# Performance work log

Measured on AMD Instinct MI355X. Metric: run time of the kernel, lower is better.

The kernel has to match this reference:

```python
import jax, jax.numpy as jnp
import numpy as np

NEG_INF = -9e15
LEAKY_SLOPE = 0.01  # PyTorch F.leaky_relu default


def setup_inputs() -> dict:
    key = jax.random.key(0)
    k1, k2, k3, k4 = jax.random.split(key, 4)
    B, N, Fin, Fout = 4, 4096, 64, 64
    X = jax.random.normal(k1, (B, N, Fin), dtype=jnp.float32)
    A = jax.random.randint(k2, (N, N), 0, 2, dtype=jnp.int32)
    weight = jax.random.normal(k3, (Fin, Fout), dtype=jnp.float32) * 0.15
    a = jax.random.normal(k4, (2 * Fout, 1), dtype=jnp.float32) * 0.15
    return {"X": X, "A": A, "weight": weight, "a": a}


def reference(X, A, weight, a):
    B, N, _ = X.shape
    Fout = weight.shape[1]
    # add self loops: A[i,i] = 1
    mask = (A > 0) | jnp.eye(N, dtype=bool)  # [N, N]
    Xw = jnp.matmul(X, weight)  # [B, N, Fout]
    # additive attention: e_ij = leaky_relu(a_l . x_i + a_r . x_j)
    # equivalent to the repeat/cat/matmul in the original, without O(N^2 F) memory
    a_l = a[:Fout, 0]   # [Fout]
    a_r = a[Fout:, 0]   # [Fout]
    left = jnp.einsum('bnf,f->bn', Xw, a_l)   # [B, N]
    right = jnp.einsum('bnf,f->bn', Xw, a_r)  # [B, N]
    e = left[:, :, None] + right[:, None, :]  # [B, N, N]
    e = jnp.where(e >= 0, e, LEAKY_SLOPE * e)
    att = jnp.where(mask[None, :, :], e, NEG_INF)
    att = jax.nn.softmax(att, axis=-1)  # dropout p=0 -> identity
    out = jnp.matmul(att, Xw)  # [B, N, Fout]
    return out
```

## Files before the change

kernel.cpp:

```cpp
#include <hip/hip_runtime.h>
#include <hip/hip_bf16.h>
#include <math.h>

#define BB 4
#define NN 4096
#define FF 64
#define KS (NN / 32)
#define NKW (KS / 4)
#define C0F 3.35462628e-4f
#define C1F 3.35462628e-6f
#define PREB 512

typedef _Float16 half8 __attribute__((ext_vector_type(8)));
typedef float f32x4 __attribute__((ext_vector_type(4)));

__global__ __launch_bounds__(256, 2)
void k_prep(const float* __restrict__ X, const float* __restrict__ W,
            const float* __restrict__ avec, const int* __restrict__ A,
            _Float16* __restrict__ XwP, float2* __restrict__ LE,
            float* __restrict__ ERt, float* __restrict__ RCt,
            unsigned int* __restrict__ bitsT) {
    __shared__ __align__(16) float Wl[64 * 64];
    __shared__ __align__(16) float Xl[32][64];
    __shared__ __align__(16) float T[32][65];
    __shared__ float al[64];
    __shared__ float ar[64];

    const int t = threadIdx.x;

    if (blockIdx.x >= PREB) {
        int pidx = (blockIdx.x - PREB) * 256 + t;
        int row  = pidx >> 10;
        int c4   = pidx & 1023;
        const uint4* A4 = (const uint4*)A;
        uint4 av = A4[pidx];
        unsigned int nib = 0;
        nib |= ((int)av.x > 0) ? 1u : 0u;
        nib |= ((int)av.y > 0) ? 2u : 0u;
        nib |= ((int)av.z > 0) ? 4u : 0u;
        nib |= ((int)av.w > 0) ? 8u : 0u;
        if (c4 == (row >> 2)) nib |= 1u << (row & 3);
        int lane = t & 63;
        unsigned int v = nib << ((lane & 7) * 4);
        v |= __shfl_xor(v, 1);
        v |= __shfl_xor(v, 2);
        v |= __shfl_xor(v, 4);
        if ((lane & 7) == 0)
            bitsT[(size_t)(c4 >> 3) * NN + row] = v;
        return;
    }

    const int lane = t & 63;
    const int wv = t >> 6;
    const int r0 = blockIdx.x * 32;

    #pragma unroll
    for (int k = 0; k < 16; ++k) Wl[t + k * 256] = W[t + k * 256];
    if (t < 64) { al[t] = avec[t]; ar[t] = avec[64 + t]; }
    {
        const float4* xs = (const float4*)(X + (size_t)r0 * 64);
        float4* xd = (float4*)&Xl[0][0];
        xd[t] = xs[t];
        xd[t + 256] = xs[t + 256];
    }
    __syncthreads();

    float Wreg[64];
    #pragma unroll
    for (int k = 0; k < 64; ++k) Wreg[k] = Wl[k * 64 + lane];

    #pragma unroll
    for (int rr = 0; rr < 8; ++rr) {
        int lrow = wv * 8 + rr;
        int row  = r0 + lrow;
        float a0 = 0.f, a1 = 0.f, a2 = 0.f, a3 = 0.f;
        #pragma unroll
        for (int k = 0; k < 64; k += 4) {
            float4 x = *(const float4*)&Xl[lrow][k];
            a0 = fmaf(x.x, Wreg[k],     a0);
            a1 = fmaf(x.y, Wreg[k + 1], a1);
            a2 = fmaf(x.z, Wreg[k + 2], a2);
            a3 = fmaf(x.w, Wreg[k + 3], a3);
        }
        float acc = (a0 + a1) + (a2 + a3);
        T[lrow][lane] = acc;

        float lv = acc * al[lane];
        float rv = acc * ar[lane];
        #pragma unroll
        for (int off = 32; off; off >>= 1) {
            lv += __shfl_xor(lv, off, 64);
            rv += __shfl_xor(rv, off, 64);
        }
        if (lane == 0) {
            LE[row]  = make_float2(lv * C1F, __expf(lv - 8.f));
            ERt[row] = __expf(rv);
            RCt[row] = fmaf(rv, C1F, C0F);
        }
    }
    __syncthreads();

    int b  = r0 >> 12;
    int ks = (r0 & (NN - 1)) >> 5;
    int ct = t >> 6;
    int q  = lane >> 4, n = lane & 15;
    half8 h;
    #pragma unroll
    for (int jj = 0; jj < 8; ++jj)
        h[jj] = (_Float16)T[q * 8 + jj][ct * 16 + n];
    *(half8*)&XwP[((((size_t)b * KS + ks) * 4 + ct) * 64 + lane) * 8] = h;
}

__global__ __launch_bounds__(256, 2)
void k_main(const _Float16* __restrict__ XwP, const float2* __restrict__ LE,
            const float* __restrict__ ERt, const float* __restrict__ RCt,
            const unsigned int* __restrict__ bitsT, float* __restrict__ out) {
    __shared__ __align__(16) char smem[32768];
    __shared__ uint2 lutm[16];
    float* REs_er = (float*)smem;
    float* REs_rc = (float*)(smem + 16384);
    float (*Lacc)[32][68] = (float (*)[32][68])smem;
    float* Lsum = (float*)(smem + 17408);

    const int t  = threadIdx.x;
    const int b  = blockIdx.y;
    const int i0 = blockIdx.x * 32;

    const int lane = t & 63;
    const int wv   = t >> 6;
    const int lm   = lane & 15;
    const int q    = lane >> 4;

    const int rowa = i0 + lm;
    const int rowb = i0 + 16 + lm;
    const float2 lea = LE[b * NN + rowa];
    const float2 leb = LE[b * NN + rowb];
    const _Float16* xp = XwP + (size_t)b * KS * 2048 + (size_t)lane * 8;

    if (t < 16)
        lutm[t] = make_uint2(((t & 1) ? 0xFFFFu : 0u) | ((t & 2) ? 0xFFFF0000u : 0u),
                             ((t & 4) ? 0xFFFFu : 0u) | ((t & 8) ? 0xFFFF0000u : 0u));

    {
        const float4* es = (const float4*)(ERt + (size_t)b * NN);
        const float4* cs = (const float4*)(RCt + (size_t)b * NN);
        float4* ed = (float4*)REs_er;
        float4* cd = (float4*)REs_rc;
        #pragma unroll
        for (int k = 0; k < 4; ++k) {
            ed[t + k * 256] = es[t + k * 256];
            cd[t + k * 256] = cs[t + k * 256];
        }
    }
    __syncthreads();

    f32x4 acca[4], accb[4];
    f32x4 sacca = (f32x4)0.f, saccb = (f32x4)0.f;
    #pragma unroll
    for (int ct = 0; ct < 4; ++ct) { acca[ct] = (f32x4)0.f; accb[ct] = (f32x4)0.f; }
    half8 vones;
    #pragma unroll
    for (int k = 0; k < 8; ++k) vones[k] = (_Float16)1.0f;

    const int ks0 = wv * NKW;

    const _Float16* base = xp + (size_t)ks0 * 2048;
    half8 nb0 = *(const half8*)(base + 0 * 512);
    half8 nb1 = *(const half8*)(base + 1 * 512);
    half8 nb2 = *(const half8*)(base + 2 * 512);
    half8 nb3 = *(const half8*)(base + 3 * 512);
    unsigned int nwa = bitsT[(size_t)ks0 * NN + rowa];
    unsigned int nwb = bitsT[(size_t)ks0 * NN + rowb];

    #pragma unroll 4
    for (int kk = 0; kk < NKW; ++kk) {
        half8 bf0 = nb0, bf1 = nb1, bf2 = nb2, bf3 = nb3;
        unsigned int wax = nwa >> (q * 8);
        unsigned int wbx = nwb >> (q * 8);
        uint2 ma0 = lutm[wax & 15], ma1 = lutm[(wax >> 4) & 15];
        uint2 mb0 = lutm[wbx & 15], mb1 = lutm[(wbx >> 4) & 15];

        {
            int nk = kk + 1 < NKW ? kk + 1 : kk;
            const _Float16* nbase = xp + (size_t)(ks0 + nk) * 2048;
            nb0 = *(const half8*)(nbase + 0 * 512);
            nb1 = *(const half8*)(nbase + 1 * 512);
            nb2 = *(const half8*)(nbase + 2 * 512);
            nb3 = *(const half8*)(nbase + 3 * 512);
            nwa = bitsT[(size_t)(ks0 + nk) * NN + rowa];
            nwb = bitsT[(size_t)(ks0 + nk) * NN + rowb];
        }

        const float4* ep = (const float4*)(REs_er + (ks0 + kk) * 32 + q * 8);
        float4 e0v = ep[0], e1v = ep[1];
        const float4* cp = (const float4*)(REs_rc + (ks0 + kk) * 32 + q * 8);
        float4 c0v = cp[0], c1v = cp[1];
        float er8[8] = {e0v.x, e0v.y, e0v.z, e0v.w, e1v.x, e1v.y, e1v.z, e1v.w};
        float rc8[8] = {c0v.x, c0v.y, c0v.z, c0v.w, c1v.x, c1v.y, c1v.z, c1v.w};

        float pa[8], pb[8];
        #pragma unroll
        for (int jj = 0; jj < 8; ++jj)
            pa[jj] = fmaxf(lea.y * er8[jj], lea.x + rc8[jj]);
        #pragma unroll
        for (int jj = 0; jj < 8; ++jj)
            pb[jj] = fmaxf(leb.y * er8[jj], leb.x + rc8[jj]);

        uint4 ua, ub;
        ua.x = __builtin_bit_cast(unsigned int, __builtin_amdgcn_cvt_pkrtz(pa[0], pa[1])) & ma0.x;
        ua.y = __builtin_bit_cast(unsigned int, __builtin_amdgcn_cvt_pkrtz(pa[2], pa[3])) & ma0.y;
        ua.z = __builtin_bit_cast(unsigned int, __builtin_amdgcn_cvt_pkrtz(pa[4], pa[5])) & ma1.x;
        ua.w = __builtin_bit_cast(unsigned int, __builtin_amdgcn_cvt_pkrtz(pa[6], pa[7])) & ma1.y;
        ub.x = __builtin_bit_cast(unsigned int, __builtin_amdgcn_cvt_pkrtz(pb[0], pb[1])) & mb0.x;
        ub.y = __builtin_bit_cast(unsigned int, __builtin_amdgcn_cvt_pkrtz(pb[2], pb[3])) & mb0.y;
        ub.z = __builtin_bit_cast(unsigned int, __builtin_amdgcn_cvt_pkrtz(pb[4], pb[5])) & mb1.x;
        ub.w = __builtin_bit_cast(unsigned int, __builtin_amdgcn_cvt_pkrtz(pb[6], pb[7])) & mb1.y;
        half8 a0a = __builtin_bit_cast(half8, ua);
        half8 a0b = __builtin_bit_cast(half8, ub);

        __builtin_amdgcn_s_setprio(1);
        acca[0] = __builtin_amdgcn_mfma_f32_16x16x32_f16(a0a, bf0, acca[0], 0, 0, 0);
        acca[1] = __builtin_amdgcn_mfma_f32_16x16x32_f16(a0a, bf1, acca[1], 0, 0, 0);
        acca[2] = __builtin_amdgcn_mfma_f32_16x16x32_f16(a0a, bf2, acca[2], 0, 0, 0);
        acca[3] = __builtin_amdgcn_mfma_f32_16x16x32_f16(a0a, bf3, acca[3], 0, 0, 0);
        sacca   = __builtin_amdgcn_mfma_f32_16x16x32_f16(a0a, vones, sacca, 0, 0, 0);

        accb[0] = __builtin_amdgcn_mfma_f32_16x16x32_f16(a0b, bf0, accb[0], 0, 0, 0);
        accb[1] = __builtin_amdgcn_mfma_f32_16x16x32_f16(a0b, bf1, accb[1], 0, 0, 0);
        accb[2] = __builtin_amdgcn_mfma_f32_16x16x32_f16(a0b, bf2, accb[2], 0, 0, 0);
        accb[3] = __builtin_amdgcn_mfma_f32_16x16x32_f16(a0b, bf3, accb[3], 0, 0, 0);
        saccb   = __builtin_amdgcn_mfma_f32_16x16x32_f16(a0b, vones, saccb, 0, 0, 0);
        __builtin_amdgcn_s_setprio(0);
    }

    __syncthreads();

    if (wv >= 2) {
        #pragma unroll
        for (int r = 0; r < 4; ++r) {
            int lrow = q * 4 + r;
            #pragma unroll
            for (int ct = 0; ct < 4; ++ct) {
                Lacc[wv - 2][lrow][ct * 16 + lm]      = acca[ct][r];
                Lacc[wv - 2][16 + lrow][ct * 16 + lm] = accb[ct][r];
            }
            if (lm == 0) {
                Lsum[(wv - 2) * 32 + lrow]      = sacca[r];
                Lsum[(wv - 2) * 32 + 16 + lrow] = saccb[r];
            }
        }
    }
    __syncthreads();
    if (wv < 2) {
        #pragma unroll
        for (int r = 0; r < 4; ++r) {
            int lrow = q * 4 + r;
            #pragma unroll
            for (int ct = 0; ct < 4; ++ct) {
                Lacc[wv][lrow][ct * 16 + lm]      += acca[ct][r];
                Lacc[wv][16 + lrow][ct * 16 + lm] += accb[ct][r];
            }
            if (lm == 0) {
                Lsum[wv * 32 + lrow]      += sacca[r];
                Lsum[wv * 32 + 16 + lrow] += saccb[r];
            }
        }
    }
    __syncthreads();
    #pragma unroll
    for (int it = 0; it < 2; ++it) {
        int idx  = t + it * 256;
        int lrow = idx >> 4;
        int c0   = (idx & 15) * 4;
        float s = Lsum[lrow] + Lsum[32 + lrow];
        float inv = 1.f / s;
        float4 o;
        o.x = (Lacc[0][lrow][c0 + 0] + Lacc[1][lrow][c0 + 0]) * inv;
        o.y = (Lacc[0][lrow][c0 + 1] + Lacc[1][lrow][c0 + 1]) * inv;
        o.z = (Lacc[0][lrow][c0 + 2] + Lacc[1][lrow][c0 + 2]) * inv;
        o.w = (Lacc[0][lrow][c0 + 3] + Lacc[1][lrow][c0 + 3]) * inv;
        *(float4*)&out[((size_t)(b * NN + i0 + lrow) << 6) + c0] = o;
    }
}

extern "C" void kernel_launch(void* const* d_in, const int* in_sizes, int n_in,
                              void* d_out, int out_size, void* d_ws, size_t ws_size,
                              hipStream_t stream) {
    const float* X    = (const float*)d_in[0];
    const int*   A    = (const int*)d_in[1];
    const float* W    = (const float*)d_in[2];
    const float* avec = (const float*)d_in[3];
    float* out = (float*)d_out;

    char* ws = (char*)d_ws;
    size_t off = 0;
    _Float16* XwP = (_Float16*)(ws + off); off += (size_t)BB * NN * FF * 2;
    float2* LE = (float2*)(ws + off);      off += (size_t)BB * NN * 8;
    float* ERt = (float*)(ws + off);       off += (size_t)BB * NN * 4;
    float* RCt = (float*)(ws + off);       off += (size_t)BB * NN * 4;
    unsigned int* bitsT = (unsigned int*)(ws + off);
    off += (size_t)KS * NN * 4;
    (void)off; (void)ws_size;

    k_prep<<<PREB + NN * NN / 1024, 256, 0, stream>>>(X, W, avec, A, XwP, LE, ERt, RCt, bitsT);
    k_main<<<dim3(NN / 32, BB), 256, 0, stream>>>(XwP, LE, ERt, RCt, bitsT, out);
}
```

Baseline: 125.6 us.

## Process 64 rows per block to reuse XwP B-fragments across four row groups

```diff
diff --git a/kernel.cpp b/kernel.cpp
--- a/kernel.cpp
+++ b/kernel.cpp
@@ -111,30 +111,33 @@
     *(half8*)&XwP[((((size_t)b * KS + ks) * 4 + ct) * 64 + lane) * 8] = h;
 }
 
-__global__ __launch_bounds__(256, 2)
+__global__ __launch_bounds__(256, 1)
 void k_main(const _Float16* __restrict__ XwP, const float2* __restrict__ LE,
             const float* __restrict__ ERt, const float* __restrict__ RCt,
             const unsigned int* __restrict__ bitsT, float* __restrict__ out) {
-    __shared__ __align__(16) char smem[32768];
+    __shared__ __align__(16) char smem[35840];
     __shared__ uint2 lutm[16];
     float* REs_er = (float*)smem;
     float* REs_rc = (float*)(smem + 16384);
-    float (*Lacc)[32][68] = (float (*)[32][68])smem;
-    float* Lsum = (float*)(smem + 17408);
+    float (*Lacc)[64][68] = (float (*)[64][68])smem;
+    float* Lsum = (float*)(smem + 34816);
 
     const int t  = threadIdx.x;
     const int b  = blockIdx.y;
-    const int i0 = blockIdx.x * 32;
+    const int i0 = blockIdx.x * 64;
 
     const int lane = t & 63;
     const int wv   = t >> 6;
     const int lm   = lane & 15;
     const int q    = lane >> 4;
 
-    const int rowa = i0 + lm;
-    const int rowb = i0 + 16 + lm;
-    const float2 lea = LE[b * NN + rowa];
-    const float2 leb = LE[b * NN + rowb];
+    int rowg[4];
+    float2 le[4];
+    #pragma unroll
+    for (int g = 0; g < 4; ++g) {
+        rowg[g] = i0 + g * 16 + lm;
+        le[g]   = LE[b * NN + rowg[g]];
+    }
     const _Float16* xp = XwP + (size_t)b * KS * 2048 + (size_t)lane * 8;
 
     if (t < 16)
@@ -154,10 +157,14 @@
     }
     __syncthreads();
 
-    f32x4 acca[4], accb[4];
-    f32x4 sacca = (f32x4)0.f, saccb = (f32x4)0.f;
-    #pragma unroll
-    for (int ct = 0; ct < 4; ++ct) { acca[ct] = (f32x4)0.f; accb[ct] = (f32x4)0.f; }
+    f32x4 acc[4][4];
+    f32x4 sacc[4];
+    #pragma unroll
+    for (int g = 0; g < 4; ++g) {
+        sacc[g] = (f32x4)0.f;
+        #pragma unroll
+        for (int ct = 0; ct < 4; ++ct) acc[g][ct] = (f32x4)0.f;
+    }
     half8 vones;
     #pragma unroll
     for (int k = 0; k < 8; ++k) vones[k] = (_Float16)1.0f;
@@ -169,16 +176,16 @@
     half8 nb1 = *(const half8*)(base + 1 * 512);
     half8 nb2 = *(const half8*)(base + 2 * 512);
     half8 nb3 = *(const half8*)(base + 3 * 512);
-    unsigned int nwa = bitsT[(size_t)ks0 * NN + rowa];
-    unsigned int nwb = bitsT[(size_t)ks0 * NN + rowb];
-
-    #pragma unroll 4
+    unsigned int nw[4];
+    #pragma unroll
+    for (int g = 0; g < 4; ++g) nw[g] = bitsT[(size_t)ks0 * NN + rowg[g]];
+
+    #pragma unroll 2
     for (int kk = 0; kk < NKW; ++kk) {
         half8 bf0 = nb0, bf1 = nb1, bf2 = nb2, bf3 = nb3;
-        unsigned int wax = nwa >> (q * 8);
-        unsigned int wbx = nwb >> (q * 8);
-        uint2 ma0 = lutm[wax & 15], ma1 = lutm[(wax >> 4) & 15];
-        uint2 mb0 = lutm[wbx & 15], mb1 = lutm[(wbx >> 4) & 15];
+        unsigned int wx[4];
+        #pragma unroll
+        for (int g = 0; g < 4; ++g) wx[g] = nw[g] >> (q * 8);
 
         {
             int nk = kk + 1 < NKW ? kk + 1 : kk;
@@ -187,8 +194,9 @@
             nb1 = *(const half8*)(nbase + 1 * 512);
             nb2 = *(const half8*)(nbase + 2 * 512);
             nb3 = *(const half8*)(nbase + 3 * 512);
-            nwa = bitsT[(size_t)(ks0 + nk) * NN + rowa];
-            nwb = bitsT[(size_t)(ks0 + nk) * NN + rowb];
+            #pragma unroll
+            for (int g = 0; g < 4; ++g)
+                nw[g] = bitsT[(size_t)(ks0 + nk) * NN + rowg[g]];
         }
 
         const float4* ep = (const float4*)(REs_er + (ks0 + kk) * 32 + q * 8);
@@ -198,81 +206,64 @@
         float er8[8] = {e0v.x, e0v.y, e0v.z, e0v.w, e1v.x, e1v.y, e1v.z, e1v.w};
         float rc8[8] = {c0v.x, c0v.y, c0v.z, c0v.w, c1v.x, c1v.y, c1v.z, c1v.w};
 
-        float pa[8], pb[8];
-        #pragma unroll
-        for (int jj = 0; jj < 8; ++jj)
-            pa[jj] = fmaxf(lea.y * er8[jj], lea.x + rc8[jj]);
-        #pragma unroll
-        for (int jj = 0; jj < 8; ++jj)
-            pb[jj] = fmaxf(leb.y * er8[jj], leb.x + rc8[jj]);
-
-        uint4 ua, ub;
-        ua.x = __builtin_bit_cast(unsigned int, __builtin_amdgcn_cvt_pkrtz(pa[0], pa[1])) & ma0.x;
-        ua.y = __builtin_bit_cast(unsigned int, __builtin_amdgcn_cvt_pkrtz(pa[2], pa[3])) & ma0.y;
-        ua.z = __builtin_bit_cast(unsigned int, __builtin_amdgcn_cvt_pkrtz(pa[4], pa[5])) & ma1.x;
-        ua.w = __builtin_bit_cast(unsigned int, __builtin_amdgcn_cvt_pkrtz(pa[6], pa[7])) & ma1.y;
-        ub.x = __builtin_bit_cast(unsigned int, __builtin_amdgcn_cvt_pkrtz(pb[0], pb[1])) & mb0.x;
-        ub.y = __builtin_bit_cast(unsigned int, __builtin_amdgcn_cvt_pkrtz(pb[2], pb[3])) & mb0.y;
-        ub.z = __builtin_bit_cast(unsigned int, __builtin_amdgcn_cvt_pkrtz(pb[4], pb[5])) & mb1.x;
-        ub.w = __builtin_bit_cast(unsigned int, __builtin_amdgcn_cvt_pkrtz(pb[6], pb[7])) & mb1.y;
-        half8 a0a = __builtin_bit_cast(half8, ua);
-        half8 a0b = __builtin_bit_cast(half8, ub);
-
-        __builtin_amdgcn_s_setprio(1);
-        acca[0] = __builtin_amdgcn_mfma_f32_16x16x32_f16(a0a, bf0, acca[0], 0, 0, 0);
-        acca[1] = __builtin_amdgcn_mfma_f32_16x16x32_f16(a0a, bf1, acca[1], 0, 0, 0);
-        acca[2] = __builtin_amdgcn_mfma_f32_16x16x32_f16(a0a, bf2, acca[2], 0, 0, 0);
-        acca[3] = __builtin_amdgcn_mfma_f32_16x16x32_f16(a0a, bf3, acca[3], 0, 0, 0);
-        sacca   = __builtin_amdgcn_mfma_f32_16x16x32_f16(a0a, vones, sacca, 0, 0, 0);
-
-        accb[0] = __builtin_amdgcn_mfma_f32_16x16x32_f16(a0b, bf0, accb[0], 0, 0, 0);
-        accb[1] = __builtin_amdgcn_mfma_f32_16x16x32_f16(a0b, bf1, accb[1], 0, 0, 0);
-        accb[2] = __builtin_amdgcn_mfma_f32_16x16x32_f16(a0b, bf2, accb[2], 0, 0, 0);
-        accb[3] = __builtin_amdgcn_mfma_f32_16x16x32_f16(a0b, bf3, accb[3], 0, 0, 0);
-        saccb   = __builtin_amdgcn_mfma_f32_16x16x32_f16(a0b, vones, saccb, 0, 0, 0);
-        __builtin_amdgcn_s_setprio(0);
+        #pragma unroll
+        for (int g = 0; g < 4; ++g) {
+            uint2 m0 = lutm[wx[g] & 15], m1 = lutm[(wx[g] >> 4) & 15];
+            float p[8];
+            #pragma unroll
+            for (int jj = 0; jj < 8; ++jj)
+                p[jj] = fmaxf(le[g].y * er8[jj], le[g].x + rc8[jj]);
+            uint4 u;
+            u.x = __builtin_bit_cast(unsigned int, __builtin_amdgcn_cvt_pkrtz(p[0], p[1])) & m0.x;
+            u.y = __builtin_bit_cast(unsigned int, __builtin_amdgcn_cvt_pkrtz(p[2], p[3])) & m0.y;
+            u.z = __builtin_bit_cast(unsigned int, __builtin_amdgcn_cvt_pkrtz(p[4], p[5])) & m1.x;
+            u.w = __builtin_bit_cast(unsigned int, __builtin_amdgcn_cvt_pkrtz(p[6], p[7])) & m1.y;
+            half8 af = __builtin_bit_cast(half8, u);
+
+            acc[g][0] = __builtin_amdgcn_mfma_f32_16x16x32_f16(af, bf0, acc[g][0], 0, 0, 0);
+            acc[g][1] = __builtin_amdgcn_mfma_f32_16x16x32_f16(af, bf1, acc[g][1], 0, 0, 0);
+            acc[g][2] = __builtin_amdgcn_mfma_f32_16x16x32_f16(af, bf2, acc[g][2], 0, 0, 0);
+            acc[g][3] = __builtin_amdgcn_mfma_f32_16x16x32_f16(af, bf3, acc[g][3], 0, 0, 0);
+            sacc[g]   = __builtin_amdgcn_mfma_f32_16x16x32_f16(af, vones, sacc[g], 0, 0, 0);
+        }
     }
 
     __syncthreads();
 
     if (wv >= 2) {
         #pragma unroll
-        for (int r = 0; r < 4; ++r) {
-            int lrow = q * 4 + r;
-            #pragma unroll
-            for (int ct = 0; ct < 4; ++ct) {
-                Lacc[wv - 2][lrow][ct * 16 + lm]      = acca[ct][r];
-                Lacc[wv - 2][16 + lrow][ct * 16 + lm] = accb[ct][r];
+        for (int g = 0; g < 4; ++g) {
+            #pragma unroll
+            for (int r = 0; r < 4; ++r) {
+                int lrow = g * 16 + q * 4 + r;
+                #pragma unroll
+                for (int ct = 0; ct < 4; ++ct)
+                    Lacc[wv - 2][lrow][ct * 16 + lm] = acc[g][ct][r];
+                if (lm == 0) Lsum[(wv - 2) * 64 + lrow] = sacc[g][r];
             }
-            if (lm == 0) {
-                Lsum[(wv - 2) * 32 + lrow]      = sacca[r];
-                Lsum[(wv - 2) * 32 + 16 + lrow] = saccb[r];
+        }
+    }
+    __syncthreads();
+    if (wv < 2) {
+        #pragma unroll
+        for (int g = 0; g < 4; ++g) {
+            #pragma unroll
+            for (int r = 0; r < 4; ++r) {
+                int lrow = g * 16 + q * 4 + r;
+                #pragma unroll
+                for (int ct = 0; ct < 4; ++ct)
+                    Lacc[wv][lrow][ct * 16 + lm] += acc[g][ct][r];
+                if (lm == 0) Lsum[wv * 64 + lrow] += sacc[g][r];
             }
         }
     }
     __syncthreads();
-    if (wv < 2) {
-        #pragma unroll
-        for (int r = 0; r < 4; ++r) {
-            int lrow = q * 4 + r;
-            #pragma unroll
-            for (int ct = 0; ct < 4; ++ct) {
-                Lacc[wv][lrow][ct * 16 + lm]      += acca[ct][r];
-                Lacc[wv][16 + lrow][ct * 16 + lm] += accb[ct][r];
-            }
-            if (lm == 0) {
-                Lsum[wv * 32 + lrow]      += sacca[r];
-                Lsum[wv * 32 + 16 + lrow] += saccb[r];
-            }
-        }
-    }
-    __syncthreads();
-    #pragma unroll
-    for (int it = 0; it < 2; ++it) {
+    #pragma unroll
+    for (int it = 0; it < 4; ++it) {
         int idx  = t + it * 256;
         int lrow = idx >> 4;
         int c0   = (idx & 15) * 4;
-        float s = Lsum[lrow] + Lsum[32 + lrow];
+        float s = Lsum[lrow] + Lsum[64 + lrow];
         float inv = 1.f / s;
         float4 o;
         o.x = (Lacc[0][lrow][c0 + 0] + Lacc[1][lrow][c0 + 0]) * inv;
@@ -303,5 +294,5 @@
     (void)off; (void)ws_size;
 
     k_prep<<<PREB + NN * NN / 1024, 256, 0, stream>>>(X, W, avec, A, XwP, LE, ERt, RCt, bitsT);
-    k_main<<<dim3(NN / 32, BB), 256, 0, stream>>>(XwP, LE, ERt, RCt, bitsT, out);
+    k_main<<<dim3(NN / 64, BB), 256, 0, stream>>>(XwP, LE, ERt, RCt, bitsT, out);
 }
```

Result: slower. 133.5 us (+6.3%).

## Deepen software pipeline to two-stage ping-pong prefetch in attention MFMA loop

Applied to the files above, without the earlier changes.

```diff
diff --git a/kernel.cpp b/kernel.cpp
--- a/kernel.cpp
+++ b/kernel.cpp
@@ -164,74 +164,101 @@
 
     const int ks0 = wv * NKW;
 
-    const _Float16* base = xp + (size_t)ks0 * 2048;
-    half8 nb0 = *(const half8*)(base + 0 * 512);
-    half8 nb1 = *(const half8*)(base + 1 * 512);
-    half8 nb2 = *(const half8*)(base + 2 * 512);
-    half8 nb3 = *(const half8*)(base + 3 * 512);
-    unsigned int nwa = bitsT[(size_t)ks0 * NN + rowa];
-    unsigned int nwb = bitsT[(size_t)ks0 * NN + rowb];
-
-    #pragma unroll 4
-    for (int kk = 0; kk < NKW; ++kk) {
-        half8 bf0 = nb0, bf1 = nb1, bf2 = nb2, bf3 = nb3;
-        unsigned int wax = nwa >> (q * 8);
-        unsigned int wbx = nwb >> (q * 8);
-        uint2 ma0 = lutm[wax & 15], ma1 = lutm[(wax >> 4) & 15];
-        uint2 mb0 = lutm[wbx & 15], mb1 = lutm[(wbx >> 4) & 15];
-
-        {
-            int nk = kk + 1 < NKW ? kk + 1 : kk;
-            const _Float16* nbase = xp + (size_t)(ks0 + nk) * 2048;
-            nb0 = *(const half8*)(nbase + 0 * 512);
-            nb1 = *(const half8*)(nbase + 1 * 512);
-            nb2 = *(const half8*)(nbase + 2 * 512);
-            nb3 = *(const half8*)(nbase + 3 * 512);
-            nwa = bitsT[(size_t)(ks0 + nk) * NN + rowa];
-            nwb = bitsT[(size_t)(ks0 + nk) * NN + rowb];
-        }
-
-        const float4* ep = (const float4*)(REs_er + (ks0 + kk) * 32 + q * 8);
-        float4 e0v = ep[0], e1v = ep[1];
-        const float4* cp = (const float4*)(REs_rc + (ks0 + kk) * 32 + q * 8);
-        float4 c0v = cp[0], c1v = cp[1];
-        float er8[8] = {e0v.x, e0v.y, e0v.z, e0v.w, e1v.x, e1v.y, e1v.z, e1v.w};
-        float rc8[8] = {c0v.x, c0v.y, c0v.z, c0v.w, c1v.x, c1v.y, c1v.z, c1v.w};
-
-        float pa[8], pb[8];
-        #pragma unroll
-        for (int jj = 0; jj < 8; ++jj)
-            pa[jj] = fmaxf(lea.y * er8[jj], lea.x + rc8[jj]);
-        #pragma unroll
-        for (int jj = 0; jj < 8; ++jj)
-            pb[jj] = fmaxf(leb.y * er8[jj], leb.x + rc8[jj]);
-
-        uint4 ua, ub;
-        ua.x = __builtin_bit_cast(unsigned int, __builtin_amdgcn_cvt_pkrtz(pa[0], pa[1])) & ma0.x;
-        ua.y = __builtin_bit_cast(unsigned int, __builtin_amdgcn_cvt_pkrtz(pa[2], pa[3])) & ma0.y;
-        ua.z = __builtin_bit_cast(unsigned int, __builtin_amdgcn_cvt_pkrtz(pa[4], pa[5])) & ma1.x;
-        ua.w = __builtin_bit_cast(unsigned int, __builtin_amdgcn_cvt_pkrtz(pa[6], pa[7])) & ma1.y;
-        ub.x = __builtin_bit_cast(unsigned int, __builtin_amdgcn_cvt_pkrtz(pb[0], pb[1])) & mb0.x;
-        ub.y = __builtin_bit_cast(unsigned int, __builtin_amdgcn_cvt_pkrtz(pb[2], pb[3])) & mb0.y;
-        ub.z = __builtin_bit_cast(unsigned int, __builtin_amdgcn_cvt_pkrtz(pb[4], pb[5])) & mb1.x;
-        ub.w = __builtin_bit_cast(unsigned int, __builtin_amdgcn_cvt_pkrtz(pb[6], pb[7])) & mb1.y;
-        half8 a0a = __builtin_bit_cast(half8, ua);
-        half8 a0b = __builtin_bit_cast(half8, ub);
-
-        __builtin_amdgcn_s_setprio(1);
-        acca[0] = __builtin_amdgcn_mfma_f32_16x16x32_f16(a0a, bf0, acca[0], 0, 0, 0);
-        acca[1] = __builtin_amdgcn_mfma_f32_16x16x32_f16(a0a, bf1, acca[1], 0, 0, 0);
-        acca[2] = __builtin_amdgcn_mfma_f32_16x16x32_f16(a0a, bf2, acca[2], 0, 0, 0);
-        acca[3] = __builtin_amdgcn_mfma_f32_16x16x32_f16(a0a, bf3, acca[3], 0, 0, 0);
-        sacca   = __builtin_amdgcn_mfma_f32_16x16x32_f16(a0a, vones, sacca, 0, 0, 0);
-
-        accb[0] = __builtin_amdgcn_mfma_f32_16x16x32_f16(a0b, bf0, accb[0], 0, 0, 0);
-        accb[1] = __builtin_amdgcn_mfma_f32_16x16x32_f16(a0b, bf1, accb[1], 0, 0, 0);
-        accb[2] = __builtin_amdgcn_mfma_f32_16x16x32_f16(a0b, bf2, accb[2], 0, 0, 0);
-        accb[3] = __builtin_amdgcn_mfma_f32_16x16x32_f16(a0b, bf3, accb[3], 0, 0, 0);
-        saccb   = __builtin_amdgcn_mfma_f32_16x16x32_f16(a0b, vones, saccb, 0, 0, 0);
-        __builtin_amdgcn_s_setprio(0);
-    }
+    half8 fA0, fA1, fA2, fA3, fB0, fB1, fB2, fB3;
+    unsigned int wAa, wAb, wBa, wBb;
+    uint2 mAa0, mAa1, mAb0, mAb1, mBa0, mBa1, mBb0, mBb1;
+    float4 eA0, eA1, cA0, cA1, eB0, eB1, cB0, cB1;
+
+    {
+        const _Float16* p0 = xp + (size_t)(ks0 + 0) * 2048;
+        fA0 = *(const half8*)(p0 + 0 * 512);
+        fA1 = *(const half8*)(p0 + 1 * 512);
+        fA2 = *(const half8*)(p0 + 2 * 512);
+        fA3 = *(const half8*)(p0 + 3 * 512);
+        wAa = bitsT[(size_t)(ks0 + 0) * NN + rowa];
+        wAb = bitsT[(size_t)(ks0 + 0) * NN + rowb];
+        const _Float16* p1 = xp + (size_t)(ks0 + 1) * 2048;
+        fB0 = *(const half8*)(p1 + 0 * 512);
+        fB1 = *(const half8*)(p1 + 1 * 512);
+        fB2 = *(const half8*)(p1 + 2 * 512);
+        fB3 = *(const half8*)(p1 + 3 * 512);
+        wBa = bitsT[(size_t)(ks0 + 1) * NN + rowa];
+        wBb = bitsT[(size_t)(ks0 + 1) * NN + rowb];
+        eA0 = *(const float4*)(REs_er + (ks0 + 0) * 32 + q * 8);
+        eA1 = *(const float4*)(REs_er + (ks0 + 0) * 32 + q * 8 + 4);
+        cA0 = *(const float4*)(REs_rc + (ks0 + 0) * 32 + q * 8);
+        cA1 = *(const float4*)(REs_rc + (ks0 + 0) * 32 + q * 8 + 4);
+        unsigned int wax = wAa >> (q * 8), wbx = wAb >> (q * 8);
+        mAa0 = lutm[wax & 15]; mAa1 = lutm[(wax >> 4) & 15];
+        mAb0 = lutm[wbx & 15]; mAb1 = lutm[(wbx >> 4) & 15];
+    }
+
+#define BODY(FE0,FE1,FE2,FE3, WXa,WXb, M_A0,M_A1,M_B0,M_B1, E0v,E1v,C0v,C1v, \
+             WOa,WOb, MO_A0,MO_A1,MO_B0,MO_B1, EO0,EO1,CO0,CO1, kn_lds, kn_vm) \
+    { \
+        unsigned int wax_ = (WOa) >> (q * 8), wbx_ = (WOb) >> (q * 8); \
+        MO_A0 = lutm[wax_ & 15]; MO_A1 = lutm[(wax_ >> 4) & 15]; \
+        MO_B0 = lutm[wbx_ & 15]; MO_B1 = lutm[(wbx_ >> 4) & 15]; \
+        EO0 = *(const float4*)(REs_er + (kn_lds) * 32 + q * 8); \
+        EO1 = *(const float4*)(REs_er + (kn_lds) * 32 + q * 8 + 4); \
+        CO0 = *(const float4*)(REs_rc + (kn_lds) * 32 + q * 8); \
+        CO1 = *(const float4*)(REs_rc + (kn_lds) * 32 + q * 8 + 4); \
+        const _Float16* nb_ = xp + (size_t)(kn_vm) * 2048; \
+        half8 t0_ = *(const half8*)(nb_ + 0 * 512); \
+        half8 t1_ = *(const half8*)(nb_ + 1 * 512); \
+        half8 t2_ = *(const half8*)(nb_ + 2 * 512); \
+        half8 t3_ = *(const half8*)(nb_ + 3 * 512); \
+        unsigned int twa_ = bitsT[(size_t)(kn_vm) * NN + rowa]; \
+        unsigned int twb_ = bitsT[(size_t)(kn_vm) * NN + rowb]; \
+        float er8[8] = {E0v.x, E0v.y, E0v.z, E0v.w, E1v.x, E1v.y, E1v.z, E1v.w}; \
+        float rc8[8] = {C0v.x, C0v.y, C0v.z, C0v.w, C1v.x, C1v.y, C1v.z, C1v.w}; \
+        float pa_[8], pb_[8]; \
+        _Pragma("unroll") \
+        for (int jj = 0; jj < 8; ++jj) pa_[jj] = fmaxf(lea.y * er8[jj], lea.x + rc8[jj]); \
+        _Pragma("unroll") \
+        for (int jj = 0; jj < 8; ++jj) pb_[jj] = fmaxf(leb.y * er8[jj], leb.x + rc8[jj]); \
+        uint4 ua_, ub_; \
+        ua_.x = __builtin_bit_cast(unsigned int, __builtin_amdgcn_cvt_pkrtz(pa_[0], pa_[1])) & M_A0.x; \
+        ua_.y = __builtin_bit_cast(unsigned int, __builtin_amdgcn_cvt_pkrtz(pa_[2], pa_[3])) & M_A0.y; \
+        ua_.z = __builtin_bit_cast(unsigned int, __builtin_amdgcn_cvt_pkrtz(pa_[4], pa_[5])) & M_A1.x; \
+        ua_.w = __builtin_bit_cast(unsigned int, __builtin_amdgcn_cvt_pkrtz(pa_[6], pa_[7])) & M_A1.y; \
+        ub_.x = __builtin_bit_cast(unsigned int, __builtin_amdgcn_cvt_pkrtz(pb_[0], pb_[1])) & M_B0.x; \
+        ub_.y = __builtin_bit_cast(unsigned int, __builtin_amdgcn_cvt_pkrtz(pb_[2], pb_[3])) & M_B0.y; \
+        ub_.z = __builtin_bit_cast(unsigned int, __builtin_amdgcn_cvt_pkrtz(pb_[4], pb_[5])) & M_B1.x; \
+        ub_.w = __builtin_bit_cast(unsigned int, __builtin_amdgcn_cvt_pkrtz(pb_[6], pb_[7])) & M_B1.y; \
+        half8 a0a_ = __builtin_bit_cast(half8, ua_); \
+        half8 a0b_ = __builtin_bit_cast(half8, ub_); \
+        __builtin_amdgcn_s_setprio(1); \
+        acca[0] = __builtin_amdgcn_mfma_f32_16x16x32_f16(a0a_, FE0, acca[0], 0, 0, 0); \
+        acca[1] = __builtin_amdgcn_mfma_f32_16x16x32_f16(a0a_, FE1, acca[1], 0, 0, 0); \
+        acca[2] = __builtin_amdgcn_mfma_f32_16x16x32_f16(a0a_, FE2, acca[2], 0, 0, 0); \
+        acca[3] = __builtin_amdgcn_mfma_f32_16x16x32_f16(a0a_, FE3, acca[3], 0, 0, 0); \
+        sacca   = __builtin_amdgcn_mfma_f32_16x16x32_f16(a0a_, vones, sacca, 0, 0, 0); \
+        accb[0] = __builtin_amdgcn_mfma_f32_16x16x32_f16(a0b_, FE0, accb[0], 0, 0, 0); \
+        accb[1] = __builtin_amdgcn_mfma_f32_16x16x32_f16(a0b_, FE1, accb[1], 0, 0, 0); \
+        accb[2] = __builtin_amdgcn_mfma_f32_16x16x32_f16(a0b_, FE2, accb[2], 0, 0, 0); \
+        accb[3] = __builtin_amdgcn_mfma_f32_16x16x32_f16(a0b_, FE3, accb[3], 0, 0, 0); \
+        saccb   = __builtin_amdgcn_mfma_f32_16x16x32_f16(a0b_, vones, saccb, 0, 0, 0); \
+        __builtin_amdgcn_s_setprio(0); \
+        FE0 = t0_; FE1 = t1_; FE2 = t2_; FE3 = t3_; \
+        WXa = twa_; WXb = twb_; \
+    }
+
+    for (int kk = 0; kk < NKW; kk += 2) {
+        int e_lds = ks0 + kk + 1;
+        int e_vm  = ks0 + (kk + 2 < NKW ? kk + 2 : NKW - 1);
+        BODY(fA0, fA1, fA2, fA3, wAa, wAb, mAa0, mAa1, mAb0, mAb1,
+             eA0, eA1, cA0, cA1,
+             wBa, wBb, mBa0, mBa1, mBb0, mBb1, eB0, eB1, cB0, cB1,
+             e_lds, e_vm);
+        int o_lds = ks0 + (kk + 2 < NKW ? kk + 2 : NKW - 1);
+        int o_vm  = ks0 + (kk + 3 < NKW ? kk + 3 : NKW - 1);
+        BODY(fB0, fB1, fB2, fB3, wBa, wBb, mBa0, mBa1, mBb0, mBb1,
+             eB0, eB1, cB0, cB1,
+             wAa, wAb, mAa0, mAa1, mAb0, mAb1, eA0, eA1, cA0, cA1,
+             o_lds, o_vm);
+    }
+#undef BODY
 
     __syncthreads();
 
```

Measured after the change: 125.9 us. About the same (+0.2%).
